# Performance work log

Measured on AMD Instinct MI355X. Metric: run time of the kernel, lower is better.

The kernel has to match this reference:

```python
import jax, jax.numpy as jnp
import numpy as np

C1 = 512  # channels1 (query input dim)
C = 512   # channels (model dim)


def setup_inputs() -> dict:
    key = jax.random.key(0)
    ks = jax.random.split(key, 12)
    B, Lq, Lk = 8, 2048, 2048
    s1 = 1.0 / np.sqrt(C1)
    s = 1.0 / np.sqrt(C)
    return {
        "rep": jax.random.normal(ks[0], (B, Lq, C1), dtype=jnp.float32),
        "rep1": jax.random.normal(ks[1], (B, Lk, C), dtype=jnp.float32),
        "Wq_w": jax.random.uniform(ks[2], (C1, C), jnp.float32, -s1, s1),
        "Wq_b": jax.random.uniform(ks[3], (C,), jnp.float32, -s1, s1),
        "Wk_w": jax.random.uniform(ks[4], (C, C), jnp.float32, -s, s),
        "Wk_b": jax.random.uniform(ks[5], (C,), jnp.float32, -s, s),
        "Wv_w": jax.random.uniform(ks[6], (C, C), jnp.float32, -s, s),
        "Wv_b": jax.random.uniform(ks[7], (C,), jnp.float32, -s, s),
        "FC_w": jax.random.uniform(ks[8], (C, C), jnp.float32, -s, s),
        "FC_b": jax.random.uniform(ks[9], (C,), jnp.float32, -s, s),
    }


def reference(rep, rep1, Wq_w, Wq_b, Wk_w, Wk_b, Wv_w, Wv_b, FC_w, FC_b):
    # Linear + ReLU projections (single head)
    q = jax.nn.relu(jnp.einsum('blc,cd->bld', rep, Wq_w) + Wq_b)    # [B,Lq,C]
    k = jax.nn.relu(jnp.einsum('blc,cd->bld', rep1, Wk_w) + Wk_b)   # [B,Lk,C]
    v = jax.nn.relu(jnp.einsum('blc,cd->bld', rep1, Wv_w) + Wv_b)   # [B,Lk,C]
    scores = jnp.einsum('bqd,bkd->bqk', q, k) / jnp.sqrt(jnp.float32(C))
    attn = jax.nn.softmax(scores, axis=-1)                           # [B,Lq,Lk]
    out = jnp.einsum('bqk,bkd->bqd', attn, v)                        # [B,Lq,C]
    out = jax.nn.relu(jnp.einsum('bld,de->ble', out, FC_w) + FC_b)
    return out
```

## Files before the change

kernel.cpp:

```cpp
#include <hip/hip_runtime.h>


typedef __attribute__((ext_vector_type(8))) short short8;
typedef __attribute__((ext_vector_type(4))) float f32x4;

#define SEQ 2048
#define CH 512
#define NB 8
#define MTOT (NB * SEQ)

#define GLDS16(gp, lp)                                                                  \
  __builtin_amdgcn_global_load_lds((const __attribute__((address_space(1))) void*)(gp), \
                                   (__attribute__((address_space(3))) void*)(lp), 16, 0, 0)

__device__ __forceinline__ unsigned short f2bf(float f) {
  unsigned u = __float_as_uint(f);
  u += 0x7fffu + ((u >> 16) & 1u);
  return (unsigned short)(u >> 16);
}

__device__ __forceinline__ unsigned pack2bf(float lo, float hi) {
  return __builtin_amdgcn_perm(__float_as_uint(hi), __float_as_uint(lo), 0x07060302u);
}

__global__ __launch_bounds__(256) void prep2_kernel(
    const float* __restrict__ W0, const float* __restrict__ W1,
    const float* __restrict__ W2, const float* __restrict__ W3,
    unsigned short* __restrict__ Wt,
    const float* __restrict__ Wk_b, const float* __restrict__ Wv_b,
    float* __restrict__ biasKV, float* __restrict__ rowsum) {
  __shared__ __attribute__((aligned(16))) unsigned short tile[64 * 72];
  const int blk = blockIdx.x;
  const int t = threadIdx.x;
  if (blk < 256) {
    const int z = blk >> 6;
    const int bx = blk & 7, by = (blk >> 3) & 7;
    const float* W = (z == 0) ? W0 : (z == 1) ? W1 : (z == 2) ? W2 : W3;
    unsigned short* Wtz = Wt + (long)z * 512 * 512;
    const int k0 = by * 64, n0 = bx * 64;
    const int r = t >> 4, cq = (t & 15) * 4;
#pragma unroll
    for (int j = 0; j < 4; ++j) {
      int row = r + 16 * j;
      float4 v = *(const float4*)&W[(long)(k0 + row) * 512 + n0 + cq];
      tile[row * 72 + cq + 0] = f2bf(v.x);
      tile[row * 72 + cq + 1] = f2bf(v.y);
      tile[row * 72 + cq + 2] = f2bf(v.z);
      tile[row * 72 + cq + 3] = f2bf(v.w);
    }
    __syncthreads();
#pragma unroll
    for (int j = 0; j < 4; ++j) {
      int row = r + 16 * j;
      ushort4 o;
      o.x = tile[(cq + 0) * 72 + row];
      o.y = tile[(cq + 1) * 72 + row];
      o.z = tile[(cq + 2) * 72 + row];
      o.w = tile[(cq + 3) * 72 + row];
      *(ushort4*)&Wtz[(long)(n0 + row) * 512 + k0 + cq] = o;
    }
  } else if (blk == 256) {
    biasKV[t] = Wk_b[t];
    biasKV[t + 256] = Wk_b[t + 256];
    biasKV[t + 512] = Wv_b[t];
    biasKV[t + 768] = Wv_b[t + 256];
  } else {
    const int zb = blk - 257;
    f32x4 z4 = {0.f, 0.f, 0.f, 0.f};
    *(f32x4*)&rowsum[(zb * 256 + t) * 4] = z4;
  }
}

template <int LDO>
__device__ __forceinline__ void proj_body(const float* __restrict__ A,
                                          const unsigned short* __restrict__ Bt,
                                          const float* __restrict__ bias,
                                          unsigned short* __restrict__ Op,
                                          long m0, long n0, unsigned short* smem) {
  float* Af = (float*)smem;
  unsigned short* Bl = smem + 8192;
  const int t = threadIdx.x;
  const int w = t >> 6, l = t & 63;
  const int wr = w >> 1, wc = w & 1;
  const int lr = l & 15, lg = l >> 4;
  const float* ga = A + (m0 + 32 * w + (l >> 3)) * CH + ((l & 7) ^ (l >> 3)) * 4;
  const unsigned short* gb =
      Bt + (n0 + 32 * w + (l >> 2)) * CH + (((l & 3) ^ ((l >> 3) & 3)) * 8);
  float* la = Af + 32 * w * 32;
  unsigned short* lb = Bl + 32 * w * 32;

  f32x4 acc[4][4] = {};
  for (int k0 = 0; k0 < CH; k0 += 32) {
#pragma unroll
    for (int j = 0; j < 4; ++j) GLDS16(ga + 8 * j * CH, la + 8 * j * 32);
    GLDS16(gb, lb);
    GLDS16(gb + 16 * CH, lb + 16 * 32);
    ga += 32; gb += 32;
    __syncthreads();
    short8 af[4], bfr[4];
#pragma unroll
    for (int i = 0; i < 4; ++i) {
      const int row = 64 * wr + 16 * i + lr;
      f32x4 a0 = *(f32x4*)&Af[row * 32 + ((2 * lg) ^ (lr & 7)) * 4];
      f32x4 a1 = *(f32x4*)&Af[row * 32 + ((2 * lg + 1) ^ (lr & 7)) * 4];
      union { unsigned u[4]; short8 s; } pk;
      pk.u[0] = pack2bf(a0[0], a0[1]);
      pk.u[1] = pack2bf(a0[2], a0[3]);
      pk.u[2] = pack2bf(a1[0], a1[1]);
      pk.u[3] = pack2bf(a1[2], a1[3]);
      af[i] = pk.s;
      bfr[i] = *(short8*)&Bl[(64 * wc + 16 * i + lr) * 32 + (lg ^ ((lr >> 1) & 3)) * 8];
    }
#pragma unroll
    for (int mi = 0; mi < 4; ++mi)
#pragma unroll
      for (int ni = 0; ni < 4; ++ni)
        acc[mi][ni] =
            __builtin_amdgcn_mfma_f32_16x16x32_bf16(af[mi], bfr[ni], acc[mi][ni], 0, 0, 0);
    __syncthreads();
  }
  unsigned short* patch = smem;
  float bv[4];
#pragma unroll
  for (int ni = 0; ni < 4; ++ni) bv[ni] = bias[n0 + 64 * wc + 16 * ni + lr];
#pragma unroll
  for (int mi = 0; mi < 4; ++mi)
#pragma unroll
    for (int ni = 0; ni < 4; ++ni)
#pragma unroll
      for (int r = 0; r < 4; ++r) {
        const int m = 64 * wr + 16 * mi + 4 * lg + r;
        const int n = 64 * wc + 16 * ni + lr;
        patch[m * 128 + ((n >> 3) ^ (m & 15)) * 8 + (n & 7)] =
            f2bf(fmaxf(acc[mi][ni][r] + bv[ni], 0.0f));
      }
  __syncthreads();
  const int q = t & 3;
#pragma unroll
  for (int p = 0; p < 2; ++p) {
    const int m = 64 * p + (t >> 2);
#pragma unroll
    for (int i = 0; i < 4; ++i) {
      const int cc = i * 4 + q;
      short8 x = *(short8*)&patch[m * 128 + ((cc ^ (m & 15)) * 8)];
      *(short8*)&Op[(m0 + m) * LDO + n0 + cc * 8] = x;
    }
  }
}

__global__ __launch_bounds__(256) void proj_kernel(const float* __restrict__ rep,
                                                   const float* __restrict__ rep1,
                                                   const unsigned short* __restrict__ Wt,
                                                   const float* __restrict__ Wq_b,
                                                   const float* __restrict__ biasKV,
                                                   unsigned short* __restrict__ Qb,
                                                   unsigned short* __restrict__ KVb) {
  __shared__ __attribute__((aligned(16))) unsigned short smem[16384];
  const long m0 = (long)blockIdx.y * 128;
  if (blockIdx.x < 4)
    proj_body<CH>(rep, Wt, Wq_b, Qb, m0, (long)blockIdx.x * 128, smem);
  else
    proj_body<1024>(rep1, Wt + 512 * 512, biasKV, KVb, m0, (long)(blockIdx.x - 4) * 128, smem);
}

template <int EPI, int LDA, int LDB, int LDO, int K, int BK>
__device__ __forceinline__ void gemm_body(const unsigned short* __restrict__ A,
                                          const unsigned short* __restrict__ Bt,
                                          const float* __restrict__ bias,
                                          float* __restrict__ rowsum,
                                          void* __restrict__ outp,
                                          long m0, long n0, unsigned short* smem) {
  unsigned short* Al = smem;
  unsigned short* Bl = smem + 128 * BK;
  const int t = threadIdx.x;
  const int w = t >> 6, l = t & 63;
  const int wr = w >> 1, wc = w & 1;
  const int lr = l & 15, lg = l >> 4;
  constexpr int NC = BK / 8;
  const int rl = l / NC, cc0 = l % NC;
  unsigned short* la = &Al[32 * w * BK];
  unsigned short* lb = &Bl[32 * w * BK];
  const int srow = 32 * w + rl;
  const int sxor = (cc0 ^ (rl & (NC - 1))) * 8;
  const unsigned short* ga = A + (m0 + srow) * (long)LDA + sxor;
  const unsigned short* gb = Bt + (n0 + srow) * (long)LDB + sxor;

  f32x4 acc[4][4] = {};
  for (int k0 = 0; k0 < K; k0 += BK) {
#pragma unroll
    for (int j = 0; j < 4; ++j) {
      GLDS16(ga + (long)8 * j * LDA, la + j * 8 * BK);
      GLDS16(gb + (long)8 * j * LDB, lb + j * 8 * BK);
    }
    ga += BK; gb += BK;
    __syncthreads();
#pragma unroll
    for (int h = 0; h < BK / 32; ++h) {
      short8 af[4], bfr[4];
#pragma unroll
      for (int i = 0; i < 4; ++i) {
        const int kc = ((h * 4 + lg) ^ (lr & (NC - 1))) * 8;
        af[i]  = *(short8*)&Al[(64 * wr + 16 * i + lr) * BK + kc];
        bfr[i] = *(short8*)&Bl[(64 * wc + 16 * i + lr) * BK + kc];
      }
#pragma unroll
      for (int mi = 0; mi < 4; ++mi)
#pragma unroll
        for (int ni = 0; ni < 4; ++ni)
          acc[mi][ni] =
              __builtin_amdgcn_mfma_f32_16x16x32_bf16(af[mi], bfr[ni], acc[mi][ni], 0, 0, 0);
    }
    __syncthreads();
  }

  if (EPI == 6 || EPI == 2) {
    unsigned short* patch = smem;
    float rsum[4][4] = {};
#pragma unroll
    for (int mi = 0; mi < 4; ++mi)
#pragma unroll
      for (int ni = 0; ni < 4; ++ni)
#pragma unroll
        for (int r = 0; r < 4; ++r) {
          const int m = 64 * wr + 16 * mi + 4 * lg + r;
          const int n = 64 * wc + 16 * ni + lr;
          float a = acc[mi][ni][r];
          unsigned short ob;
          if (EPI == 6) ob = f2bf(a);
          else {
            float p = exp2f(a * 0.06375872f);
            ob = f2bf(p);
            rsum[mi][r] += __uint_as_float((unsigned)ob << 16);
          }
          patch[m * 128 + ((n >> 3) ^ (m & 15)) * 8 + (n & 7)] = ob;
        }
    __syncthreads();
    unsigned short* O = (unsigned short*)outp;
    const int q = t & 3;
#pragma unroll
    for (int p = 0; p < 2; ++p) {
      const int m = 64 * p + (t >> 2);
#pragma unroll
      for (int i = 0; i < 4; ++i) {
        const int cc = i * 4 + q;
        short8 x = *(short8*)&patch[m * 128 + ((cc ^ (m & 15)) * 8)];
        *(short8*)&O[(m0 + m) * LDO + n0 + cc * 8] = x;
      }
    }
    if (EPI == 2) {
#pragma unroll
      for (int off = 1; off < 16; off <<= 1)
#pragma unroll
        for (int mi = 0; mi < 4; ++mi)
#pragma unroll
          for (int r = 0; r < 4; ++r) rsum[mi][r] += __shfl_xor(rsum[mi][r], off);
      if (lr == 0) {
#pragma unroll
        for (int mi = 0; mi < 4; ++mi)
#pragma unroll
          for (int r = 0; r < 4; ++r)
            atomicAdd(&rowsum[m0 + 64 * wr + 16 * mi + 4 * lg + r], rsum[mi][r]);
      }
    }
  } else {
    float* patchF = (float*)smem;
    float bv[4];
#pragma unroll
    for (int ni = 0; ni < 4; ++ni) bv[ni] = bias[n0 + 64 * wc + 16 * ni + lr];
    float inv[4][4];
#pragma unroll
    for (int mi = 0; mi < 4; ++mi)
#pragma unroll
      for (int r = 0; r < 4; ++r)
        inv[mi][r] = 1.0f / rowsum[m0 + 64 * wr + 16 * mi + 4 * lg + r];
#pragma unroll
    for (int mi = 0; mi < 4; ++mi)
#pragma unroll
      for (int ni = 0; ni < 4; ++ni)
#pragma unroll
        for (int r = 0; r < 4; ++r) {
          const int m = 64 * wr + 16 * mi + 4 * lg + r;
          const int n = 64 * wc + 16 * ni + lr;
          patchF[m * 128 + ((n >> 2) ^ (m & 31)) * 4 + (n & 3)] =
              fmaxf(acc[mi][ni][r] * inv[mi][r] + bv[ni], 0.0f);
        }
    __syncthreads();
    float* O = (float*)outp;
    const int q = t & 3;
#pragma unroll
    for (int p = 0; p < 2; ++p) {
      const int m = 64 * p + (t >> 2);
#pragma unroll
      for (int i = 0; i < 8; ++i) {
        const int cc = i * 4 + q;
        f32x4 x = *(f32x4*)&patchF[m * 128 + ((cc ^ (m & 31)) * 4)];
        *(f32x4*)&O[(m0 + m) * LDO + n0 + cc * 4] = x;
      }
    }
  }
}

__global__ __launch_bounds__(256) void qkvf_kernel(const unsigned short* __restrict__ Qb,
                                                   const unsigned short* __restrict__ KVb,
                                                   const unsigned short* __restrict__ WtF,
                                                   float* __restrict__ rowsum,
                                                   unsigned short* __restrict__ Pbuf,
                                                   unsigned short* __restrict__ VFt) {
  __shared__ __attribute__((aligned(16))) unsigned short smem[2 * 128 * 64];
  const int bz = blockIdx.z;
  if (blockIdx.y < 16) {
    gemm_body<2, CH, 1024, SEQ, CH, 64>(
        Qb + (long)bz * SEQ * CH, KVb + (long)bz * SEQ * 1024, nullptr,
        rowsum + (long)bz * SEQ, Pbuf + (long)bz * SEQ * SEQ,
        (long)blockIdx.y * 128, (long)blockIdx.x * 128, smem);
  } else {
    gemm_body<6, CH, 1024, SEQ, CH, 64>(
        WtF, KVb + 512 + (long)bz * SEQ * 1024, nullptr, nullptr,
        VFt + (long)bz * CH * SEQ,
        (long)(blockIdx.y - 16) * 128, (long)blockIdx.x * 128, smem);
  }
}

__global__ __launch_bounds__(256) void pvf_kernel(const unsigned short* __restrict__ Pbuf,
                                                  const unsigned short* __restrict__ VFt,
                                                  const float* __restrict__ FC_b,
                                                  float* __restrict__ rowsum,
                                                  float* __restrict__ out) {
  __shared__ __attribute__((aligned(16))) unsigned short smem[32768];
  const int bz = blockIdx.z;
  gemm_body<5, SEQ, SEQ, CH, SEQ, 64>(
      Pbuf + (long)bz * SEQ * SEQ, VFt + (long)bz * CH * SEQ, FC_b,
      rowsum + (long)bz * SEQ, out + (long)bz * SEQ * CH,
      (long)blockIdx.y * 128, (long)blockIdx.x * 128, smem);
}

extern "C" void kernel_launch(void* const* d_in, const int* in_sizes, int n_in,
                              void* d_out, int out_size, void* d_ws, size_t ws_size,
                              hipStream_t stream) {
  const float* rep  = (const float*)d_in[0];
  const float* rep1 = (const float*)d_in[1];
  const float* Wq_w = (const float*)d_in[2];
  const float* Wq_b = (const float*)d_in[3];
  const float* Wk_w = (const float*)d_in[4];
  const float* Wk_b = (const float*)d_in[5];
  const float* Wv_w = (const float*)d_in[6];
  const float* Wv_b = (const float*)d_in[7];
  const float* FC_w = (const float*)d_in[8];
  const float* FC_b = (const float*)d_in[9];
  float* out = (float*)d_out;
  char* ws = (char*)d_ws;

  const size_t MB = 1024 * 1024;
  unsigned short* Qb     = (unsigned short*)(ws + 0 * MB);
  unsigned short* KVb    = (unsigned short*)(ws + 16 * MB);
  unsigned short* VFt    = (unsigned short*)(ws + 48 * MB);
  unsigned short* Wt4    = (unsigned short*)(ws + 64 * MB);
  float*          biasKV = (float*)(ws + 66 * MB);
  unsigned short* Pbuf   = (unsigned short*)(ws + 67 * MB);
  float*          rowsum = (float*)(ws + 131 * MB);
  const size_t need = 132 * MB;
  if (ws_size < need) return;

  unsigned short* WtF = Wt4 + 3 * 512 * 512;

  prep2_kernel<<<273, 256, 0, stream>>>(Wq_w, Wk_w, Wv_w, FC_w, Wt4, Wk_b, Wv_b,
                                        biasKV, rowsum);

  proj_kernel<<<dim3(12, 128), 256, 0, stream>>>(rep, rep1, Wt4, Wq_b, biasKV, Qb, KVb);

  qkvf_kernel<<<dim3(16, 20, 8), 256, 0, stream>>>(Qb, KVb, WtF, rowsum, Pbuf, VFt);

  pvf_kernel<<<dim3(4, 16, 8), 256, 0, stream>>>(Pbuf, VFt, FC_b, rowsum, out);
}
```

Baseline: 298.7 us.

## Rewrite QK/VF GEMM as 256x256-tile 8-wave kernel with explicit LDS pipelining

Replaces the 128x128 gemm_body used for the score/exp and V·FC stages with a new 256x256-tile kernel on 512 threads. It double-buffers LDS through global_load_lds, interleaves LDS reads and MFMA quadrants between explicit barriers, and raises wave priority around the MFMAs. The larger tile is meant to improve operand reuse and hide memory latency. In exchange it uses 128KB of LDS, far more registers, and a grid of only 640 blocks, which may limit occupancy. The old EPI 2/6 epilogue is dropped from gemm_body.

```diff
diff --git a/kernel.cpp b/kernel.cpp
--- a/kernel.cpp
+++ b/kernel.cpp
@@ -213,56 +213,7 @@
     __syncthreads();
   }
 
-  if (EPI == 6 || EPI == 2) {
-    unsigned short* patch = smem;
-    float rsum[4][4] = {};
-#pragma unroll
-    for (int mi = 0; mi < 4; ++mi)
-#pragma unroll
-      for (int ni = 0; ni < 4; ++ni)
-#pragma unroll
-        for (int r = 0; r < 4; ++r) {
-          const int m = 64 * wr + 16 * mi + 4 * lg + r;
-          const int n = 64 * wc + 16 * ni + lr;
-          float a = acc[mi][ni][r];
-          unsigned short ob;
-          if (EPI == 6) ob = f2bf(a);
-          else {
-            float p = exp2f(a * 0.06375872f);
-            ob = f2bf(p);
-            rsum[mi][r] += __uint_as_float((unsigned)ob << 16);
-          }
-          patch[m * 128 + ((n >> 3) ^ (m & 15)) * 8 + (n & 7)] = ob;
-        }
-    __syncthreads();
-    unsigned short* O = (unsigned short*)outp;
-    const int q = t & 3;
-#pragma unroll
-    for (int p = 0; p < 2; ++p) {
-      const int m = 64 * p + (t >> 2);
-#pragma unroll
-      for (int i = 0; i < 4; ++i) {
-        const int cc = i * 4 + q;
-        short8 x = *(short8*)&patch[m * 128 + ((cc ^ (m & 15)) * 8)];
-        *(short8*)&O[(m0 + m) * LDO + n0 + cc * 8] = x;
-      }
-    }
-    if (EPI == 2) {
-#pragma unroll
-      for (int off = 1; off < 16; off <<= 1)
-#pragma unroll
-        for (int mi = 0; mi < 4; ++mi)
-#pragma unroll
-          for (int r = 0; r < 4; ++r) rsum[mi][r] += __shfl_xor(rsum[mi][r], off);
-      if (lr == 0) {
-#pragma unroll
-        for (int mi = 0; mi < 4; ++mi)
-#pragma unroll
-          for (int r = 0; r < 4; ++r)
-            atomicAdd(&rowsum[m0 + 64 * wr + 16 * mi + 4 * lg + r], rsum[mi][r]);
-      }
-    }
-  } else {
+  {
     float* patchF = (float*)smem;
     float bv[4];
 #pragma unroll
@@ -300,24 +251,207 @@
   }
 }
 
-__global__ __launch_bounds__(256) void qkvf_kernel(const unsigned short* __restrict__ Qb,
-                                                   const unsigned short* __restrict__ KVb,
-                                                   const unsigned short* __restrict__ WtF,
-                                                   float* __restrict__ rowsum,
-                                                   unsigned short* __restrict__ Pbuf,
-                                                   unsigned short* __restrict__ VFt) {
-  __shared__ __attribute__((aligned(16))) unsigned short smem[2 * 128 * 64];
+#define CFENCE asm volatile("" ::: "memory")
+#define SB0 __builtin_amdgcn_sched_barrier(0)
+#define BAR8                          \
+  do {                                \
+    CFENCE;                           \
+    __builtin_amdgcn_s_barrier();     \
+    SB0;                              \
+  } while (0)
+#define LGKM0                                            \
+  do {                                                   \
+    asm volatile("s_waitcnt lgkmcnt(0)" ::: "memory");   \
+    SB0;                                                 \
+  } while (0)
+#define VMC(n)                                              \
+  do {                                                      \
+    asm volatile("s_waitcnt vmcnt(" #n ")" ::: "memory");   \
+    SB0;                                                    \
+  } while (0)
+
+template <int EPI, int LDA, int LDB, int LDO, int K>
+__device__ __forceinline__ void gemm256_body(const unsigned short* __restrict__ A,
+                                             const unsigned short* __restrict__ Bt,
+                                             float* __restrict__ rowsum,
+                                             unsigned short* __restrict__ Op,
+                                             long m0, long n0,
+                                             unsigned short (*smem)[2][16384]) {
+  const int t = threadIdx.x;
+  const int w = t >> 6, l = t & 63;
+  const int wr = w >> 2, wc = w & 3;
+  const int lr = l & 15, lg = l >> 4;
+  const int srow = t >> 3;
+  const int schk = ((t & 7) ^ ((t >> 3) & 7)) * 8;
+  const unsigned short* gA = A + (m0 + srow) * (long)LDA + schk;
+  const unsigned short* gB = Bt + (n0 + srow) * (long)LDB + schk;
+
+  auto stageA = [&](int c, int half, int kt) {
+    unsigned short* d = &smem[c][0][(128 * half + 8 * w) * 64];
+    const unsigned short* g = gA + (long)(128 * half) * LDA + (long)kt * 64;
+    GLDS16(g, d);
+    GLDS16(g + (long)64 * LDA, d + 64 * 64);
+  };
+  auto stageB = [&](int c, int half, int kt) {
+    unsigned short* d = &smem[c][1][(128 * half + 8 * w) * 64];
+    const unsigned short* g = gB + (long)(128 * half) * LDB + (long)kt * 64;
+    GLDS16(g, d);
+    GLDS16(g + (long)64 * LDB, d + 64 * 64);
+  };
+
+  const int kx0 = (lg ^ (lr & 7)) * 8;
+  const int kx1 = ((4 + lg) ^ (lr & 7)) * 8;
+  short8 af[8], bf0[4], bf1[4];
+  f32x4 acc[8][4] = {};
+
+  auto readA = [&](int c, int mh) {
+#pragma unroll
+    for (int i = 0; i < 4; ++i) {
+      const unsigned short* p = &smem[c][0][(128 * wr + 16 * (4 * mh + i) + lr) * 64];
+      af[2 * i]     = *(const short8*)&p[kx0];
+      af[2 * i + 1] = *(const short8*)&p[kx1];
+    }
+  };
+  auto readB = [&](int c, int nh, short8* bf) {
+#pragma unroll
+    for (int i = 0; i < 2; ++i) {
+      const unsigned short* p = &smem[c][1][(64 * wc + 16 * (2 * nh + i) + lr) * 64];
+      bf[2 * i]     = *(const short8*)&p[kx0];
+      bf[2 * i + 1] = *(const short8*)&p[kx1];
+    }
+  };
+  auto quad = [&](int mh, int nh, const short8* bf) {
+    __builtin_amdgcn_s_setprio(1);
+#pragma unroll
+    for (int i = 0; i < 4; ++i)
+#pragma unroll
+      for (int j = 0; j < 2; ++j) {
+        acc[4 * mh + i][2 * nh + j] = __builtin_amdgcn_mfma_f32_16x16x32_bf16(
+            af[2 * i], bf[2 * j], acc[4 * mh + i][2 * nh + j], 0, 0, 0);
+        acc[4 * mh + i][2 * nh + j] = __builtin_amdgcn_mfma_f32_16x16x32_bf16(
+            af[2 * i + 1], bf[2 * j + 1], acc[4 * mh + i][2 * nh + j], 0, 0, 0);
+      }
+    __builtin_amdgcn_s_setprio(0);
+  };
+
+  stageA(0, 0, 0); stageA(0, 1, 0);
+  stageB(0, 0, 0); stageB(0, 1, 0);
+  stageB(1, 0, 1); stageB(1, 1, 1);
+  VMC(4);
+  BAR8;
+
+  constexpr int NT = K / 64;
+#pragma unroll
+  for (int it = 0; it < NT / 2; ++it) {
+    const int O = 2 * it + 1, N2 = 2 * it + 2, N3 = 2 * it + 3;
+    const bool sN2 = (N2 < NT), sN3 = (N3 < NT);
+    readA(0, 0); readB(0, 0, bf0);
+    stageA(1, 0, O);
+    BAR8; LGKM0; quad(0, 0, bf0); BAR8;
+
+    readB(0, 1, bf1);
+    stageA(1, 1, O);
+    BAR8; LGKM0; quad(0, 1, bf1); BAR8;
+
+    readA(0, 1);
+    if (sN2) stageB(0, 0, N2);
+    BAR8; LGKM0; quad(1, 1, bf1); BAR8;
+
+    if (sN2) { stageB(0, 1, N2); VMC(4); } else { VMC(0); }
+    BAR8; quad(1, 0, bf0); BAR8;
+    readA(1, 0); readB(1, 0, bf0);
+    if (sN2) stageA(0, 0, N2);
+    BAR8; LGKM0; quad(0, 0, bf0); BAR8;
+
+    readB(1, 1, bf1);
+    if (sN2) stageA(0, 1, N2);
+    BAR8; LGKM0; quad(0, 1, bf1); BAR8;
+
+    readA(1, 1);
+    if (sN3) stageB(1, 0, N3);
+    BAR8; LGKM0; quad(1, 1, bf1); BAR8;
+
+    if (sN3) { stageB(1, 1, N3); VMC(4); } else { VMC(0); }
+    BAR8; quad(1, 0, bf0); BAR8;
+  }
+
+  __syncthreads();
+  unsigned short* patch = &smem[0][0][0];
+  float rsum[8][4];
+  if (EPI == 2) {
+#pragma unroll
+    for (int mi = 0; mi < 8; ++mi)
+#pragma unroll
+      for (int r = 0; r < 4; ++r) rsum[mi][r] = 0.f;
+  }
+#pragma unroll
+  for (int mi = 0; mi < 8; ++mi)
+#pragma unroll
+    for (int ni = 0; ni < 4; ++ni)
+#pragma unroll
+      for (int r = 0; r < 4; ++r) {
+        const int m = 128 * wr + 16 * mi + 4 * lg + r;
+        const int n = 64 * wc + 16 * ni + lr;
+        const float a = acc[mi][ni][r];
+        unsigned short ob;
+        if (EPI == 6) {
+          ob = f2bf(a);
+        } else {
+          float p = exp2f(a * 0.06375872f);
+          ob = f2bf(p);
+          rsum[mi][r] += __uint_as_float((unsigned)ob << 16);
+        }
+        patch[m * 256 + (((n >> 3) ^ (m & 31)) * 8) + (n & 7)] = ob;
+      }
+  __syncthreads();
+  {
+    const int q = t & 3, mr = t >> 2;
+#pragma unroll
+    for (int p2 = 0; p2 < 2; ++p2) {
+      const int m = 128 * p2 + mr;
+#pragma unroll
+      for (int i = 0; i < 8; ++i) {
+        const int cc = i * 4 + q;
+        short8 x = *(short8*)&patch[m * 256 + ((cc ^ (m & 31)) * 8)];
+        *(short8*)&Op[(m0 + m) * (long)LDO + n0 + cc * 8] = x;
+      }
+    }
+  }
+  if (EPI == 2) {
+#pragma unroll
+    for (int off = 1; off < 16; off <<= 1)
+#pragma unroll
+      for (int mi = 0; mi < 8; ++mi)
+#pragma unroll
+        for (int r = 0; r < 4; ++r) rsum[mi][r] += __shfl_xor(rsum[mi][r], off);
+    if (lr == 0) {
+#pragma unroll
+      for (int mi = 0; mi < 8; ++mi)
+#pragma unroll
+        for (int r = 0; r < 4; ++r)
+          atomicAdd(&rowsum[m0 + 128 * wr + 16 * mi + 4 * lg + r], rsum[mi][r]);
+    }
+  }
+}
+
+__global__ __launch_bounds__(512, 2) void qkvf_kernel(const unsigned short* __restrict__ Qb,
+                                                      const unsigned short* __restrict__ KVb,
+                                                      const unsigned short* __restrict__ WtF,
+                                                      float* __restrict__ rowsum,
+                                                      unsigned short* __restrict__ Pbuf,
+                                                      unsigned short* __restrict__ VFt) {
+  __shared__ __attribute__((aligned(16))) unsigned short smem[2][2][16384];
   const int bz = blockIdx.z;
-  if (blockIdx.y < 16) {
-    gemm_body<2, CH, 1024, SEQ, CH, 64>(
-        Qb + (long)bz * SEQ * CH, KVb + (long)bz * SEQ * 1024, nullptr,
+  if (blockIdx.y < 8) {
+    gemm256_body<2, CH, 1024, SEQ, CH>(
+        Qb + (long)bz * SEQ * CH, KVb + (long)bz * SEQ * 1024,
         rowsum + (long)bz * SEQ, Pbuf + (long)bz * SEQ * SEQ,
-        (long)blockIdx.y * 128, (long)blockIdx.x * 128, smem);
+        (long)blockIdx.y * 256, (long)blockIdx.x * 256, smem);
   } else {
-    gemm_body<6, CH, 1024, SEQ, CH, 64>(
-        WtF, KVb + 512 + (long)bz * SEQ * 1024, nullptr, nullptr,
-        VFt + (long)bz * CH * SEQ,
-        (long)(blockIdx.y - 16) * 128, (long)blockIdx.x * 128, smem);
+    gemm256_body<6, CH, 1024, SEQ, CH>(
+        WtF, KVb + 512 + (long)bz * SEQ * 1024,
+        nullptr, VFt + (long)bz * CH * SEQ,
+        (long)(blockIdx.y - 8) * 256, (long)blockIdx.x * 256, smem);
   }
 }
 
@@ -368,7 +502,7 @@
 
   proj_kernel<<<dim3(12, 128), 256, 0, stream>>>(rep, rep1, Wt4, Wq_b, biasKV, Qb, KVb);
 
-  qkvf_kernel<<<dim3(16, 20, 8), 256, 0, stream>>>(Qb, KVb, WtF, rowsum, Pbuf, VFt);
+  qkvf_kernel<<<dim3(8, 10, 8), 512, 0, stream>>>(Qb, KVb, WtF, rowsum, Pbuf, VFt);
 
   pvf_kernel<<<dim3(4, 16, 8), 256, 0, stream>>>(Pbuf, VFt, FC_b, rowsum, out);
 }
```

Result: no change. 300.2 us (+0.5%).

## Rewrite PV-FC GEMM kernel with triple-buffered pipelined 256x128 tiles

Applied to the files above, without the earlier changes.

Replaces the generic gemm_body use for the P·V·FC stage with a dedicated 512-thread kernel computing 256x128 tiles. It uses a three-stage direct-to-LDS load ring with explicit vmcnt/lgkmcnt waits, barriers and MFMA priority boosts. The split-N fragment reads are meant to overlap global loads, LDS reads and matrix ops. Block indices are remapped so blocks sharing rows land on the same XCD for L2 reuse. The shared gemm epilogue drops the now-unused fp32 branch. Fewer, larger blocks may reduce latency hiding if scheduling is imperfect.

```diff
diff --git a/kernel.cpp b/kernel.cpp
--- a/kernel.cpp
+++ b/kernel.cpp
@@ -213,89 +213,52 @@
     __syncthreads();
   }
 
-  if (EPI == 6 || EPI == 2) {
-    unsigned short* patch = smem;
-    float rsum[4][4] = {};
-#pragma unroll
-    for (int mi = 0; mi < 4; ++mi)
-#pragma unroll
-      for (int ni = 0; ni < 4; ++ni)
-#pragma unroll
-        for (int r = 0; r < 4; ++r) {
-          const int m = 64 * wr + 16 * mi + 4 * lg + r;
-          const int n = 64 * wc + 16 * ni + lr;
-          float a = acc[mi][ni][r];
-          unsigned short ob;
-          if (EPI == 6) ob = f2bf(a);
-          else {
-            float p = exp2f(a * 0.06375872f);
-            ob = f2bf(p);
-            rsum[mi][r] += __uint_as_float((unsigned)ob << 16);
-          }
-          patch[m * 128 + ((n >> 3) ^ (m & 15)) * 8 + (n & 7)] = ob;
+  unsigned short* patch = smem;
+  float rsum[4][4] = {};
+#pragma unroll
+  for (int mi = 0; mi < 4; ++mi)
+#pragma unroll
+    for (int ni = 0; ni < 4; ++ni)
+#pragma unroll
+      for (int r = 0; r < 4; ++r) {
+        const int m = 64 * wr + 16 * mi + 4 * lg + r;
+        const int n = 64 * wc + 16 * ni + lr;
+        float a = acc[mi][ni][r];
+        unsigned short ob;
+        if (EPI == 6) ob = f2bf(a);
+        else {
+          float p = exp2f(a * 0.06375872f);
+          ob = f2bf(p);
+          rsum[mi][r] += __uint_as_float((unsigned)ob << 16);
         }
-    __syncthreads();
-    unsigned short* O = (unsigned short*)outp;
-    const int q = t & 3;
-#pragma unroll
-    for (int p = 0; p < 2; ++p) {
-      const int m = 64 * p + (t >> 2);
-#pragma unroll
-      for (int i = 0; i < 4; ++i) {
-        const int cc = i * 4 + q;
-        short8 x = *(short8*)&patch[m * 128 + ((cc ^ (m & 15)) * 8)];
-        *(short8*)&O[(m0 + m) * LDO + n0 + cc * 8] = x;
-      }
-    }
-    if (EPI == 2) {
-#pragma unroll
-      for (int off = 1; off < 16; off <<= 1)
-#pragma unroll
-        for (int mi = 0; mi < 4; ++mi)
-#pragma unroll
-          for (int r = 0; r < 4; ++r) rsum[mi][r] += __shfl_xor(rsum[mi][r], off);
-      if (lr == 0) {
-#pragma unroll
-        for (int mi = 0; mi < 4; ++mi)
-#pragma unroll
-          for (int r = 0; r < 4; ++r)
-            atomicAdd(&rowsum[m0 + 64 * wr + 16 * mi + 4 * lg + r], rsum[mi][r]);
-      }
-    }
-  } else {
-    float* patchF = (float*)smem;
-    float bv[4];
-#pragma unroll
-    for (int ni = 0; ni < 4; ++ni) bv[ni] = bias[n0 + 64 * wc + 16 * ni + lr];
-    float inv[4][4];
-#pragma unroll
-    for (int mi = 0; mi < 4; ++mi)
-#pragma unroll
-      for (int r = 0; r < 4; ++r)
-        inv[mi][r] = 1.0f / rowsum[m0 + 64 * wr + 16 * mi + 4 * lg + r];
-#pragma unroll
-    for (int mi = 0; mi < 4; ++mi)
-#pragma unroll
-      for (int ni = 0; ni < 4; ++ni)
-#pragma unroll
-        for (int r = 0; r < 4; ++r) {
-          const int m = 64 * wr + 16 * mi + 4 * lg + r;
-          const int n = 64 * wc + 16 * ni + lr;
-          patchF[m * 128 + ((n >> 2) ^ (m & 31)) * 4 + (n & 3)] =
-              fmaxf(acc[mi][ni][r] * inv[mi][r] + bv[ni], 0.0f);
-        }
-    __syncthreads();
-    float* O = (float*)outp;
-    const int q = t & 3;
-#pragma unroll
-    for (int p = 0; p < 2; ++p) {
-      const int m = 64 * p + (t >> 2);
-#pragma unroll
-      for (int i = 0; i < 8; ++i) {
-        const int cc = i * 4 + q;
-        f32x4 x = *(f32x4*)&patchF[m * 128 + ((cc ^ (m & 31)) * 4)];
-        *(f32x4*)&O[(m0 + m) * LDO + n0 + cc * 4] = x;
-      }
+        patch[m * 128 + ((n >> 3) ^ (m & 15)) * 8 + (n & 7)] = ob;
+      }
+  __syncthreads();
+  unsigned short* O = (unsigned short*)outp;
+  const int q = t & 3;
+#pragma unroll
+  for (int p = 0; p < 2; ++p) {
+    const int m = 64 * p + (t >> 2);
+#pragma unroll
+    for (int i = 0; i < 4; ++i) {
+      const int cc = i * 4 + q;
+      short8 x = *(short8*)&patch[m * 128 + ((cc ^ (m & 15)) * 8)];
+      *(short8*)&O[(m0 + m) * LDO + n0 + cc * 8] = x;
+    }
+  }
+  if (EPI == 2) {
+#pragma unroll
+    for (int off = 1; off < 16; off <<= 1)
+#pragma unroll
+      for (int mi = 0; mi < 4; ++mi)
+#pragma unroll
+        for (int r = 0; r < 4; ++r) rsum[mi][r] += __shfl_xor(rsum[mi][r], off);
+    if (lr == 0) {
+#pragma unroll
+      for (int mi = 0; mi < 4; ++mi)
+#pragma unroll
+        for (int r = 0; r < 4; ++r)
+          atomicAdd(&rowsum[m0 + 64 * wr + 16 * mi + 4 * lg + r], rsum[mi][r]);
     }
   }
 }
@@ -321,17 +284,156 @@
   }
 }
 
-__global__ __launch_bounds__(256) void pvf_kernel(const unsigned short* __restrict__ Pbuf,
-                                                  const unsigned short* __restrict__ VFt,
-                                                  const float* __restrict__ FC_b,
-                                                  float* __restrict__ rowsum,
-                                                  float* __restrict__ out) {
-  __shared__ __attribute__((aligned(16))) unsigned short smem[32768];
-  const int bz = blockIdx.z;
-  gemm_body<5, SEQ, SEQ, CH, SEQ, 64>(
-      Pbuf + (long)bz * SEQ * SEQ, VFt + (long)bz * CH * SEQ, FC_b,
-      rowsum + (long)bz * SEQ, out + (long)bz * SEQ * CH,
-      (long)blockIdx.y * 128, (long)blockIdx.x * 128, smem);
+#define CFENCE asm volatile("" ::: "memory")
+#define SB0 __builtin_amdgcn_sched_barrier(0)
+#define BAR8                          \
+  do {                                \
+    CFENCE;                           \
+    __builtin_amdgcn_s_barrier();     \
+    SB0;                              \
+  } while (0)
+#define LGKM0                                            \
+  do {                                                   \
+    asm volatile("s_waitcnt lgkmcnt(0)" ::: "memory");   \
+    SB0;                                                 \
+  } while (0)
+#define VMC(n)                                              \
+  do {                                                      \
+    asm volatile("s_waitcnt vmcnt(" #n ")" ::: "memory");   \
+    SB0;                                                    \
+  } while (0)
+
+__global__ __launch_bounds__(512, 2) void pvf_kernel(const unsigned short* __restrict__ Pbuf,
+                                                     const unsigned short* __restrict__ VFt,
+                                                     const float* __restrict__ FC_b,
+                                                     float* __restrict__ rowsum,
+                                                     float* __restrict__ out) {
+  __shared__ __attribute__((aligned(16))) unsigned short smem[3][24576];
+  const int s = blockIdx.x;
+  const int xcd = s & 7, j = s >> 3;
+  const int x = j & 3, pg = j >> 2;
+  const int y = xcd, bz = pg;
+  const long m0 = (long)y * 256, n0 = (long)x * 128;
+
+  const unsigned short* A  = Pbuf + (long)bz * SEQ * SEQ;
+  const unsigned short* Bt = VFt + (long)bz * CH * SEQ;
+  constexpr int LDA = SEQ, LDB = SEQ;
+  constexpr int NT = SEQ / 64;
+
+  const int t = threadIdx.x;
+  const int w = t >> 6, l = t & 63;
+  const int wr = w >> 1, wc = w & 1;
+  const int lr = l & 15, lg = l >> 4;
+
+  const int srow = t >> 3;
+  const int schk = ((t & 7) ^ ((t >> 3) & 7)) * 8;
+  const unsigned short* gA = A + (m0 + srow) * (long)LDA + schk;
+  const unsigned short* gB = Bt + (n0 + srow) * (long)LDB + schk;
+
+  auto stageA = [&](int c, int kt) {
+#pragma unroll
+    for (int jj = 0; jj < 4; ++jj) {
+      unsigned short* d = &smem[c][(64 * jj + 8 * w) * 64];
+      GLDS16(gA + (long)(64 * jj) * LDA + (long)kt * 64, d);
+    }
+  };
+  auto stageB = [&](int c, int kt) {
+#pragma unroll
+    for (int jj = 0; jj < 2; ++jj) {
+      unsigned short* d = &smem[c][16384 + (64 * jj + 8 * w) * 64];
+      GLDS16(gB + (long)(64 * jj) * LDB + (long)kt * 64, d);
+    }
+  };
+
+  const int kx0 = (lg ^ (lr & 7)) * 8;
+  const int kx1 = ((4 + lg) ^ (lr & 7)) * 8;
+  short8 af[8], bf0[4], bf1[4];
+  f32x4 acc[4][4] = {};
+
+  auto readA = [&](int c) {
+#pragma unroll
+    for (int i = 0; i < 4; ++i) {
+      const unsigned short* p = &smem[c][(64 * wr + 16 * i + lr) * 64];
+      af[2 * i]     = *(const short8*)&p[kx0];
+      af[2 * i + 1] = *(const short8*)&p[kx1];
+    }
+  };
+  auto readB = [&](int c, int nh, short8* bf) {
+#pragma unroll
+    for (int i = 0; i < 2; ++i) {
+      const unsigned short* p = &smem[c][16384 + (64 * wc + 16 * (2 * nh + i) + lr) * 64];
+      bf[2 * i]     = *(const short8*)&p[kx0];
+      bf[2 * i + 1] = *(const short8*)&p[kx1];
+    }
+  };
+  auto quad = [&](int nh, const short8* bf) {
+    __builtin_amdgcn_s_setprio(1);
+#pragma unroll
+    for (int mi = 0; mi < 4; ++mi)
+#pragma unroll
+      for (int jj = 0; jj < 2; ++jj) {
+        acc[mi][2 * nh + jj] = __builtin_amdgcn_mfma_f32_16x16x32_bf16(
+            af[2 * mi], bf[2 * jj], acc[mi][2 * nh + jj], 0, 0, 0);
+        acc[mi][2 * nh + jj] = __builtin_amdgcn_mfma_f32_16x16x32_bf16(
+            af[2 * mi + 1], bf[2 * jj + 1], acc[mi][2 * nh + jj], 0, 0, 0);
+      }
+    __builtin_amdgcn_s_setprio(0);
+  };
+
+  stageA(0, 0); stageB(0, 0);
+  stageA(1, 1); stageB(1, 1);
+  VMC(6);
+  BAR8;
+
+#pragma unroll
+  for (int kt = 0; kt < NT; ++kt) {
+    const int b = kt % 3, nb = (kt + 2) % 3;
+    const bool st = (kt + 2) < NT;
+    readA(b); readB(b, 0, bf0);
+    if (st) stageA(nb, kt + 2);
+    BAR8; LGKM0; quad(0, bf0); BAR8;
+    readB(b, 1, bf1);
+    if (st) { stageB(nb, kt + 2); VMC(6); } else { VMC(0); }
+    BAR8; LGKM0; quad(1, bf1); BAR8;
+  }
+
+  __syncthreads();
+  float* patchF = (float*)&smem[0][0];
+  float bv[4];
+#pragma unroll
+  for (int ni = 0; ni < 4; ++ni) bv[ni] = FC_b[n0 + 64 * wc + 16 * ni + lr];
+  float inv[4][4];
+#pragma unroll
+  for (int mi = 0; mi < 4; ++mi)
+#pragma unroll
+    for (int r = 0; r < 4; ++r)
+      inv[mi][r] = 1.0f / rowsum[(long)bz * SEQ + m0 + 64 * wr + 16 * mi + 4 * lg + r];
+#pragma unroll
+  for (int mi = 0; mi < 4; ++mi)
+#pragma unroll
+    for (int ni = 0; ni < 4; ++ni)
+#pragma unroll
+      for (int r = 0; r < 4; ++r) {
+        const int m = 64 * wr + 16 * mi + 4 * lg + r;
+        const int n = 64 * wc + 16 * ni + lr;
+        patchF[m * 128 + ((n >> 2) ^ (m & 31)) * 4 + (n & 3)] =
+            fmaxf(acc[mi][ni][r] * inv[mi][r] + bv[ni], 0.0f);
+      }
+  __syncthreads();
+  {
+    float* O = out + (long)bz * SEQ * CH;
+    const int q = t & 3, mr = t >> 2;
+#pragma unroll
+    for (int p2 = 0; p2 < 2; ++p2) {
+      const int m = 128 * p2 + mr;
+#pragma unroll
+      for (int i = 0; i < 8; ++i) {
+        const int cc = i * 4 + q;
+        f32x4 v = *(f32x4*)&patchF[m * 128 + ((cc ^ (m & 31)) * 4)];
+        *(f32x4*)&O[(m0 + m) * CH + n0 + cc * 4] = v;
+      }
+    }
+  }
 }
 
 extern "C" void kernel_launch(void* const* d_in, const int* in_sizes, int n_in,
@@ -370,5 +472,5 @@
 
   qkvf_kernel<<<dim3(16, 20, 8), 256, 0, stream>>>(Qb, KVb, WtF, rowsum, Pbuf, VFt);
 
-  pvf_kernel<<<dim3(4, 16, 8), 256, 0, stream>>>(Pbuf, VFt, FC_b, rowsum, out);
-}
+  pvf_kernel<<<256, 512, 0, stream>>>(Pbuf, VFt, FC_b, rowsum, out);
+}
```

After: 291.6 us. 2.4% less time.
